# Kernel optimization log

Measured on AMD Instinct MI355X. Metric: run time of the kernel, lower is better.

The kernel has to match this reference:

```python
import jax, jax.numpy as jnp
import numpy as np

B, T, D, UNITS = 64, 2048, 512, 512


def setup_inputs() -> dict:
    key = jax.random.key(0)
    ks = jax.random.split(key, 6)
    scale = 1.0 / np.sqrt(D)
    return {
        "features": jax.random.normal(ks[0], (B, T, D), dtype=jnp.float32),
        "hidden": jax.random.normal(ks[1], (B, D), dtype=jnp.float32),
        "W1_w": jax.random.normal(ks[2], (D, UNITS), dtype=jnp.float32) * scale,
        "W1_b": jnp.zeros((UNITS,), dtype=jnp.float32),
        "W2_w": jax.random.normal(ks[3], (D, UNITS), dtype=jnp.float32) * scale,
        "W2_b": jnp.zeros((UNITS,), dtype=jnp.float32),
        "V_w": jax.random.normal(ks[4], (UNITS, 1), dtype=jnp.float32) * (1.0 / np.sqrt(UNITS)),
        "V_b": jnp.zeros((1,), dtype=jnp.float32),
    }


def reference(features, hidden, W1_w, W1_b, W2_w, W2_b, V_w, V_b):
    # features: [B, T, D], hidden: [B, D]
    f_proj = jnp.einsum("btd,du->btu", features, W1_w) + W1_b      # [B, T, U]
    h_proj = (hidden @ W2_w + W2_b)[:, None, :]                     # [B, 1, U]
    score = jnp.tanh(f_proj + h_proj) @ V_w + V_b                   # [B, T, 1]
    attn = jax.nn.softmax(score, axis=1)                            # softmax over time
    context = jnp.sum(attn * features, axis=1)                      # [B, D]
    return context
```

## Files before the change

kernel.cpp:

```cpp
#include <hip/hip_runtime.h>
#include <hip/hip_bf16.h>

#define B_DIM 64
#define T_DIM 2048
#define D_DIM 512
#define U_DIM 512

typedef __bf16 bf16x8 __attribute__((ext_vector_type(8)));
typedef float  f32x4  __attribute__((ext_vector_type(4)));
typedef unsigned int u32;

__device__ __forceinline__ void gl_lds16(const __bf16* g, __bf16* l) {
    __builtin_amdgcn_global_load_lds(
        (const __attribute__((address_space(1))) u32*)g,
        (__attribute__((address_space(3))) u32*)l,
        16, 0, 0);
}

__global__ void w1s_kernel(const float* __restrict__ W1w, __bf16* __restrict__ w1s) {
    __shared__ float tile[64][33];
    const int tid = threadIdx.x;
    const int kb2 = blockIdx.x;
    const int ub  = blockIdx.y;
    #pragma unroll
    for (int i = 0; i < 8; ++i) {
        int k = i * 4 + (tid >> 6);
        int u = tid & 63;
        tile[u][k] = W1w[(kb2 * 32 + k) * U_DIM + ub * 64 + u];
    }
    __syncthreads();
    int u_l = tid >> 2;
    int kp  = (tid & 3) * 8;
    bf16x8 w;
    #pragma unroll
    for (int j = 0; j < 8; ++j) w[j] = (__bf16)tile[u_l][kp + j];
    *reinterpret_cast<bf16x8*>(&w1s[kb2 * 16384 + (ub * 64 + u_l) * 32 + kp]) = w;
}

__global__ void hproj_kernel(const float* __restrict__ hidden,
                             const float* __restrict__ W2w,
                             const float* __restrict__ W2b,
                             const float* __restrict__ W1b,
                             float* __restrict__ hp) {
    int b = blockIdx.x;
    int u = blockIdx.y * 256 + threadIdx.x;
    float acc = W2b[u] + W1b[u];
    const float* hrow = hidden + b * D_DIM;
    #pragma unroll 8
    for (int d = 0; d < D_DIM; ++d)
        acc = fmaf(hrow[d], W2w[d * U_DIM + u], acc);
    hp[b * U_DIM + u] = acc;
}

__global__ __launch_bounds__(256, 2) void score_kernel(
        const float*  __restrict__ features,
        const __bf16* __restrict__ w1s,
        const float*  __restrict__ hp,
        const float*  __restrict__ Vw,
        float*        __restrict__ scores) {
    __shared__ __align__(16) __bf16 As0[64 * 32];
    __shared__ __align__(16) __bf16 As1[64 * 32];
    __shared__ __align__(16) __bf16 Bs0[512 * 32];
    __shared__ __align__(16) __bf16 Bs1[512 * 32];
    __shared__ float red[4 * 64];

    const int tid  = threadIdx.x;
    const int row0 = blockIdx.x * 64;
    const int b    = row0 >> 11;

    const int wn   = tid >> 6;
    const int lane = tid & 63;
    const int l16  = lane & 15;
    const int quad = lane >> 4;

    const int arow = tid >> 2;
    const int aq   = tid & 3;

    f32x4 acc[4][8];
    #pragma unroll
    for (int i = 0; i < 4; ++i)
        #pragma unroll
        for (int j = 0; j < 8; ++j)
            acc[i][j] = (f32x4)0.0f;

    const float* ag = features + (size_t)(row0 + arow) * D_DIM + aq * 8;

    for (int ko = 0; ko < 8; ++ko) {
        const __bf16* bsrc0 = w1s + (2 * ko) * 16384 + tid * 8;
        const __bf16* bsrc1 = w1s + (2 * ko + 1) * 16384 + tid * 8;
        #pragma unroll
        for (int c = 0; c < 8; ++c) {
            gl_lds16(bsrc0 + c * 2048, Bs0 + c * 2048 + tid * 8);
            gl_lds16(bsrc1 + c * 2048, Bs1 + c * 2048 + tid * 8);
        }
        {
            const float4* s0 = reinterpret_cast<const float4*>(ag + ko * 64);
            const float4* s1 = reinterpret_cast<const float4*>(ag + ko * 64 + 32);
            float4 v0 = s0[0], v1 = s0[1];
            float4 v2 = s1[0], v3 = s1[1];
            bf16x8 w0, w1;
            w0[0] = (__bf16)v0.x; w0[1] = (__bf16)v0.y; w0[2] = (__bf16)v0.z; w0[3] = (__bf16)v0.w;
            w0[4] = (__bf16)v1.x; w0[5] = (__bf16)v1.y; w0[6] = (__bf16)v1.z; w0[7] = (__bf16)v1.w;
            w1[0] = (__bf16)v2.x; w1[1] = (__bf16)v2.y; w1[2] = (__bf16)v2.z; w1[3] = (__bf16)v2.w;
            w1[4] = (__bf16)v3.x; w1[5] = (__bf16)v3.y; w1[6] = (__bf16)v3.z; w1[7] = (__bf16)v3.w;
            *reinterpret_cast<bf16x8*>(&As0[arow * 32 + aq * 8]) = w0;
            *reinterpret_cast<bf16x8*>(&As1[arow * 32 + aq * 8]) = w1;
        }
        __syncthreads();

        #pragma unroll
        for (int ks = 0; ks < 2; ++ks) {
            const __bf16* Ap = ks ? As1 : As0;
            const __bf16* Bp = ks ? Bs1 : Bs0;
            bf16x8 af[4], bfr[8];
            #pragma unroll
            for (int mt = 0; mt < 4; ++mt)
                af[mt] = *reinterpret_cast<const bf16x8*>(
                    &Ap[(mt * 16 + l16) * 32 + quad * 8]);
            #pragma unroll
            for (int nt = 0; nt < 8; ++nt)
                bfr[nt] = *reinterpret_cast<const bf16x8*>(
                    &Bp[(wn * 128 + nt * 16 + l16) * 32 + quad * 8]);
            #pragma unroll
            for (int mt = 0; mt < 4; ++mt)
                #pragma unroll
                for (int nt = 0; nt < 8; ++nt)
                    acc[mt][nt] = __builtin_amdgcn_mfma_f32_16x16x32_bf16(
                        af[mt], bfr[nt], acc[mt][nt], 0, 0, 0);
        }
        __syncthreads();
    }

    float hpv[8], vwv[8];
    #pragma unroll
    for (int nt = 0; nt < 8; ++nt) {
        int u = wn * 128 + nt * 16 + l16;
        hpv[nt] = hp[b * U_DIM + u];
        vwv[nt] = Vw[u];
    }
    #pragma unroll
    for (int mt = 0; mt < 4; ++mt) {
        #pragma unroll
        for (int reg = 0; reg < 4; ++reg) {
            float s = 0.0f;
            #pragma unroll
            for (int nt = 0; nt < 8; ++nt) {
                float x = acc[mt][nt][reg] + hpv[nt];
                float e = exp2f(x * 2.88539008f);
                float th = 1.0f - 2.0f * __builtin_amdgcn_rcpf(e + 1.0f);
                s = fmaf(th, vwv[nt], s);
            }
            s += __shfl_xor(s, 1);
            s += __shfl_xor(s, 2);
            s += __shfl_xor(s, 4);
            s += __shfl_xor(s, 8);
            if (l16 == 0)
                red[wn * 64 + mt * 16 + quad * 4 + reg] = s;
        }
    }
    __syncthreads();
    if (tid < 64)
        scores[row0 + tid] = red[tid] + red[64 + tid] + red[128 + tid] + red[192 + tid];
}

__global__ void softmax_kernel(const float* __restrict__ scores, float* __restrict__ attn) {
    int b = blockIdx.x;
    int tid = threadIdx.x;
    __shared__ float red[4], red2[4];

    float s[8];
    float m = -1e30f;
    #pragma unroll
    for (int i = 0; i < 8; ++i) {
        s[i] = scores[b * T_DIM + i * 256 + tid];
        m = fmaxf(m, s[i]);
    }
    #pragma unroll
    for (int off = 1; off < 64; off <<= 1) m = fmaxf(m, __shfl_xor(m, off));
    if ((tid & 63) == 0) red[tid >> 6] = m;
    __syncthreads();
    m = fmaxf(fmaxf(red[0], red[1]), fmaxf(red[2], red[3]));

    float e[8], sum = 0.0f;
    #pragma unroll
    for (int i = 0; i < 8; ++i) {
        e[i] = exp2f((s[i] - m) * 1.44269504f);
        sum += e[i];
    }
    #pragma unroll
    for (int off = 1; off < 64; off <<= 1) sum += __shfl_xor(sum, off);
    if ((tid & 63) == 0) red2[tid >> 6] = sum;
    __syncthreads();
    sum = red2[0] + red2[1] + red2[2] + red2[3];
    float inv = 1.0f / sum;
    #pragma unroll
    for (int i = 0; i < 8; ++i)
        attn[b * T_DIM + i * 256 + tid] = e[i] * inv;
}

__global__ void context_kernel(const float* __restrict__ attn,
                               const float* __restrict__ features,
                               float* __restrict__ out) {
    __shared__ float4 red[256];
    const int tid = threadIdx.x;
    const int b   = blockIdx.y;
    const int d4  = (blockIdx.x << 5) + (tid & 31);
    const int tp  = tid >> 5;

    const float4* f  = reinterpret_cast<const float4*>(features) + (size_t)b * T_DIM * 128;
    const float*  ar = attn + b * T_DIM;

    float4 acc = {0.f, 0.f, 0.f, 0.f};
    #pragma unroll 8
    for (int i = 0; i < 256; ++i) {
        int t = tp * 256 + i;
        float a = ar[t];
        float4 v = f[(size_t)t * 128 + d4];
        acc.x = fmaf(a, v.x, acc.x);
        acc.y = fmaf(a, v.y, acc.y);
        acc.z = fmaf(a, v.z, acc.z);
        acc.w = fmaf(a, v.w, acc.w);
    }
    red[tid] = acc;
    __syncthreads();
    if (tp == 0) {
        float4 s = red[tid];
        #pragma unroll
        for (int j = 1; j < 8; ++j) {
            float4 v = red[tid + 32 * j];
            s.x += v.x; s.y += v.y; s.z += v.z; s.w += v.w;
        }
        reinterpret_cast<float4*>(out)[b * 128 + d4] = s;
    }
}

extern "C" void kernel_launch(void* const* d_in, const int* in_sizes, int n_in,
                              void* d_out, int out_size, void* d_ws, size_t ws_size,
                              hipStream_t stream) {
    const float* features = (const float*)d_in[0];
    const float* hidden   = (const float*)d_in[1];
    const float* W1w      = (const float*)d_in[2];
    const float* W1b      = (const float*)d_in[3];
    const float* W2w      = (const float*)d_in[4];
    const float* W2b      = (const float*)d_in[5];
    const float* Vw       = (const float*)d_in[6];

    char* ws = (char*)d_ws;
    __bf16* w1s    = (__bf16*)ws;
    float*  scores = (float*)(ws + (512u << 10));
    float*  attn   = (float*)(ws + (1024u << 10));
    float*  hp     = (float*)(ws + (1536u << 10));

    hipLaunchKernelGGL(w1s_kernel, dim3(16, 8), dim3(256), 0, stream, W1w, w1s);
    hipLaunchKernelGGL(hproj_kernel, dim3(B_DIM, 2), dim3(256), 0, stream,
                       hidden, W2w, W2b, W1b, hp);
    hipLaunchKernelGGL(score_kernel, dim3(2048), dim3(256), 0, stream,
                       features, w1s, hp, Vw, scores);
    hipLaunchKernelGGL(softmax_kernel, dim3(B_DIM), dim3(256), 0, stream, scores, attn);
    hipLaunchKernelGGL(context_kernel, dim3(4, B_DIM), dim3(256), 0, stream,
                       attn, features, (float*)d_out);
}
```

Before: 497.3 us.

## Reorganize W1 and A tiles into k-octet layout, halve LDS footprint, widen context grid

The weight preprocessing now stores W1 as k-octets of 8 bf16 per unit, and the score kernel stages one 32-wide K slice per iteration (16 iterations) instead of two. This halves LDS use, which can allow higher occupancy, and the octet-major layout gives conflict-free 16-byte LDS reads for the MFMA fragments. The feature load is also issued before the async weight copy. Separately, the context kernel uses 8 blocks per batch, each covering 16 float4 columns with 16 time partitions, to expose more parallelism. The cost is twice as many barriers per tile and more strided, partially coalesced feature reads.

Result: slower. 511.2 us (+2.8%).

```diff
diff --git a/kernel.cpp b/kernel.cpp
--- a/kernel.cpp
+++ b/kernel.cpp
@@ -17,24 +17,15 @@
         16, 0, 0);
 }
 
-__global__ void w1s_kernel(const float* __restrict__ W1w, __bf16* __restrict__ w1s) {
-    __shared__ float tile[64][33];
-    const int tid = threadIdx.x;
-    const int kb2 = blockIdx.x;
-    const int ub  = blockIdx.y;
-    #pragma unroll
-    for (int i = 0; i < 8; ++i) {
-        int k = i * 4 + (tid >> 6);
-        int u = tid & 63;
-        tile[u][k] = W1w[(kb2 * 32 + k) * U_DIM + ub * 64 + u];
-    }
-    __syncthreads();
-    int u_l = tid >> 2;
-    int kp  = (tid & 3) * 8;
+__global__ void w1c_kernel(const float* __restrict__ W1w, __bf16* __restrict__ w1c) {
+    int idx = blockIdx.x * 256 + threadIdx.x;
+    int u   = idx & 511;
+    int oct = idx >> 9;
     bf16x8 w;
     #pragma unroll
-    for (int j = 0; j < 8; ++j) w[j] = (__bf16)tile[u_l][kp + j];
-    *reinterpret_cast<bf16x8*>(&w1s[kb2 * 16384 + (ub * 64 + u_l) * 32 + kp]) = w;
+    for (int j = 0; j < 8; ++j)
+        w[j] = (__bf16)W1w[(oct * 8 + j) * U_DIM + u];
+    *reinterpret_cast<bf16x8*>(&w1c[(oct * 512 + (u ^ 0)) * 8]) = w;
 }
 
 __global__ void hproj_kernel(const float* __restrict__ hidden,
@@ -54,14 +45,12 @@
 
 __global__ __launch_bounds__(256, 2) void score_kernel(
         const float*  __restrict__ features,
-        const __bf16* __restrict__ w1s,
+        const __bf16* __restrict__ w1c,
         const float*  __restrict__ hp,
         const float*  __restrict__ Vw,
         float*        __restrict__ scores) {
-    __shared__ __align__(16) __bf16 As0[64 * 32];
-    __shared__ __align__(16) __bf16 As1[64 * 32];
-    __shared__ __align__(16) __bf16 Bs0[512 * 32];
-    __shared__ __align__(16) __bf16 Bs1[512 * 32];
+    __shared__ __align__(16) __bf16 Bs[4 * 512 * 8];
+    __shared__ __align__(16) __bf16 As[4 * 64 * 8];
     __shared__ float red[4 * 64];
 
     const int tid  = threadIdx.x;
@@ -73,9 +62,6 @@
     const int l16  = lane & 15;
     const int quad = lane >> 4;
 
-    const int arow = tid >> 2;
-    const int aq   = tid & 3;
-
     f32x4 acc[4][8];
     #pragma unroll
     for (int i = 0; i < 4; ++i)
@@ -83,51 +69,42 @@
         for (int j = 0; j < 8; ++j)
             acc[i][j] = (f32x4)0.0f;
 
-    const float* ag = features + (size_t)(row0 + arow) * D_DIM + aq * 8;
-
-    for (int ko = 0; ko < 8; ++ko) {
-        const __bf16* bsrc0 = w1s + (2 * ko) * 16384 + tid * 8;
-        const __bf16* bsrc1 = w1s + (2 * ko + 1) * 16384 + tid * 8;
-        #pragma unroll
-        for (int c = 0; c < 8; ++c) {
-            gl_lds16(bsrc0 + c * 2048, Bs0 + c * 2048 + tid * 8);
-            gl_lds16(bsrc1 + c * 2048, Bs1 + c * 2048 + tid * 8);
-        }
+    const float* ag = features + (size_t)(row0 + (tid & 63)) * D_DIM + (tid >> 6) * 8;
+    __bf16* as_dst = &As[tid * 8];
+
+    for (int ko = 0; ko < 16; ++ko) {
+        const float4* asrc = reinterpret_cast<const float4*>(ag + ko * 32);
+        float4 v0 = asrc[0];
+        float4 v1 = asrc[1];
+
+        const __bf16* bsrc = w1c + ko * 16384 + tid * 8;
+        #pragma unroll
+        for (int c = 0; c < 8; ++c)
+            gl_lds16(bsrc + c * 2048, Bs + c * 2048 + tid * 8);
+
         {
-            const float4* s0 = reinterpret_cast<const float4*>(ag + ko * 64);
-            const float4* s1 = reinterpret_cast<const float4*>(ag + ko * 64 + 32);
-            float4 v0 = s0[0], v1 = s0[1];
-            float4 v2 = s1[0], v3 = s1[1];
-            bf16x8 w0, w1;
-            w0[0] = (__bf16)v0.x; w0[1] = (__bf16)v0.y; w0[2] = (__bf16)v0.z; w0[3] = (__bf16)v0.w;
-            w0[4] = (__bf16)v1.x; w0[5] = (__bf16)v1.y; w0[6] = (__bf16)v1.z; w0[7] = (__bf16)v1.w;
-            w1[0] = (__bf16)v2.x; w1[1] = (__bf16)v2.y; w1[2] = (__bf16)v2.z; w1[3] = (__bf16)v2.w;
-            w1[4] = (__bf16)v3.x; w1[5] = (__bf16)v3.y; w1[6] = (__bf16)v3.z; w1[7] = (__bf16)v3.w;
-            *reinterpret_cast<bf16x8*>(&As0[arow * 32 + aq * 8]) = w0;
-            *reinterpret_cast<bf16x8*>(&As1[arow * 32 + aq * 8]) = w1;
+            bf16x8 w;
+            w[0] = (__bf16)v0.x; w[1] = (__bf16)v0.y; w[2] = (__bf16)v0.z; w[3] = (__bf16)v0.w;
+            w[4] = (__bf16)v1.x; w[5] = (__bf16)v1.y; w[6] = (__bf16)v1.z; w[7] = (__bf16)v1.w;
+            *reinterpret_cast<bf16x8*>(as_dst) = w;
         }
         __syncthreads();
 
-        #pragma unroll
-        for (int ks = 0; ks < 2; ++ks) {
-            const __bf16* Ap = ks ? As1 : As0;
-            const __bf16* Bp = ks ? Bs1 : Bs0;
-            bf16x8 af[4], bfr[8];
-            #pragma unroll
-            for (int mt = 0; mt < 4; ++mt)
-                af[mt] = *reinterpret_cast<const bf16x8*>(
-                    &Ap[(mt * 16 + l16) * 32 + quad * 8]);
+        bf16x8 af[4], bfr[8];
+        #pragma unroll
+        for (int mt = 0; mt < 4; ++mt)
+            af[mt] = *reinterpret_cast<const bf16x8*>(
+                &As[(quad * 64 + mt * 16 + l16) * 8]);
+        #pragma unroll
+        for (int nt = 0; nt < 8; ++nt)
+            bfr[nt] = *reinterpret_cast<const bf16x8*>(
+                &Bs[(quad * 512 + wn * 128 + nt * 16 + l16) * 8]);
+        #pragma unroll
+        for (int mt = 0; mt < 4; ++mt)
             #pragma unroll
             for (int nt = 0; nt < 8; ++nt)
-                bfr[nt] = *reinterpret_cast<const bf16x8*>(
-                    &Bp[(wn * 128 + nt * 16 + l16) * 32 + quad * 8]);
-            #pragma unroll
-            for (int mt = 0; mt < 4; ++mt)
-                #pragma unroll
-                for (int nt = 0; nt < 8; ++nt)
-                    acc[mt][nt] = __builtin_amdgcn_mfma_f32_16x16x32_bf16(
-                        af[mt], bfr[nt], acc[mt][nt], 0, 0, 0);
-        }
+                acc[mt][nt] = __builtin_amdgcn_mfma_f32_16x16x32_bf16(
+                    af[mt], bfr[nt], acc[mt][nt], 0, 0, 0);
         __syncthreads();
     }
 
@@ -204,16 +181,16 @@
     __shared__ float4 red[256];
     const int tid = threadIdx.x;
     const int b   = blockIdx.y;
-    const int d4  = (blockIdx.x << 5) + (tid & 31);
-    const int tp  = tid >> 5;
+    const int d4  = (blockIdx.x << 4) + (tid & 15);
+    const int tp  = tid >> 4;
 
     const float4* f  = reinterpret_cast<const float4*>(features) + (size_t)b * T_DIM * 128;
     const float*  ar = attn + b * T_DIM;
 
     float4 acc = {0.f, 0.f, 0.f, 0.f};
     #pragma unroll 8
-    for (int i = 0; i < 256; ++i) {
-        int t = tp * 256 + i;
+    for (int i = 0; i < 128; ++i) {
+        int t = tp * 128 + i;
         float a = ar[t];
         float4 v = f[(size_t)t * 128 + d4];
         acc.x = fmaf(a, v.x, acc.x);
@@ -226,8 +203,8 @@
     if (tp == 0) {
         float4 s = red[tid];
         #pragma unroll
-        for (int j = 1; j < 8; ++j) {
-            float4 v = red[tid + 32 * j];
+        for (int j = 1; j < 16; ++j) {
+            float4 v = red[tid + 16 * j];
             s.x += v.x; s.y += v.y; s.z += v.z; s.w += v.w;
         }
         reinterpret_cast<float4*>(out)[b * 128 + d4] = s;
@@ -246,17 +223,17 @@
     const float* Vw       = (const float*)d_in[6];
 
     char* ws = (char*)d_ws;
-    __bf16* w1s    = (__bf16*)ws;
+    __bf16* w1c    = (__bf16*)ws;
     float*  scores = (float*)(ws + (512u << 10));
     float*  attn   = (float*)(ws + (1024u << 10));
     float*  hp     = (float*)(ws + (1536u << 10));
 
-    hipLaunchKernelGGL(w1s_kernel, dim3(16, 8), dim3(256), 0, stream, W1w, w1s);
+    hipLaunchKernelGGL(w1c_kernel, dim3(128), dim3(256), 0, stream, W1w, w1c);
     hipLaunchKernelGGL(hproj_kernel, dim3(B_DIM, 2), dim3(256), 0, stream,
                        hidden, W2w, W2b, W1b, hp);
     hipLaunchKernelGGL(score_kernel, dim3(2048), dim3(256), 0, stream,
-                       features, w1s, hp, Vw, scores);
+                       features, w1c, hp, Vw, scores);
     hipLaunchKernelGGL(softmax_kernel, dim3(B_DIM), dim3(256), 0, stream, scores, attn);
-    hipLaunchKernelGGL(context_kernel, dim3(4, B_DIM), dim3(256), 0, stream,
+    hipLaunchKernelGGL(context_kernel, dim3(8, B_DIM), dim3(256), 0, stream,
                        attn, features, (float*)d_out);
 }
```
